# Optimization experiments

Measured on AMD Instinct MI355X. Metric: run time of the kernel, lower is better.

## Reference

```python
import jax, jax.numpy as jnp
import numpy as np

N_NODES = 10000
N_EDGES = 640000
D = 128


def setup_inputs() -> dict:
    key = jax.random.key(0)
    k1, k2, k3, k4 = jax.random.split(key, 4)
    X = jax.random.normal(k1, (N_NODES, D), dtype=jnp.float32)
    Y = jax.random.normal(k2, (N_EDGES, D), dtype=jnp.float32)
    # nn.Linear(in, out, bias=False): weight shape (out, in), y = Y @ W.T
    W = jax.random.normal(k3, (D, D), dtype=jnp.float32) * (1.0 / np.sqrt(D))
    edge_index = jax.random.randint(k4, (N_EDGES, 2), 0, N_NODES, dtype=jnp.int64)
    return {"X": X, "Y": Y, "W": W, "edge_index": edge_index}


def reference(X, Y, W, edge_index):
    # Edge transform: (E, d_in) @ (d_in, d_out) -> (E, d_out)
    Y_prime = jnp.einsum('ei,oi->eo', Y, W)
    # Scatter-add transformed edge features to source nodes
    src = edge_index[:, 0]
    agg = jax.ops.segment_sum(Y_prime, src, num_segments=X.shape[0])  # (N, d_out)
    # Residual + activation
    X_prime = jax.nn.relu(X + agg)
    return (X_prime, Y_prime)
```

## Files before the change

### kernel.cpp

```cpp
#include <hip/hip_runtime.h>

#define N_NODES 10000
#define N_EDGES 640000
#define DD 128
#define MAIN_BLOCKS 6250

typedef __attribute__((ext_vector_type(8))) short short8;
typedef __attribute__((ext_vector_type(8))) float f32x8;
typedef __attribute__((ext_vector_type(4))) float f32x4;
typedef __attribute__((ext_vector_type(2))) float f32x2;

__device__ __forceinline__ unsigned pack_bf2(float lo, float hi) {
  return __builtin_amdgcn_perm(__float_as_uint(hi), __float_as_uint(lo), 0x07060302u);
}

__device__ __forceinline__ void stage_w512(const float* __restrict__ W,
                                           short8* lwr) {
  const int tid = threadIdx.x;
#pragma unroll
  for (int t = 0; t < 4; ++t) {
    int s = t * 512 + tid;
    f32x8 v = *(const f32x8*)(W + (size_t)s * 8);
    short8 av;
    unsigned* au = (unsigned*)&av;
    au[0] = pack_bf2(v[0], v[1]);
    au[1] = pack_bf2(v[2], v[3]);
    au[2] = pack_bf2(v[4], v[5]);
    au[3] = pack_bf2(v[6], v[7]);
    int j = s >> 4;
    int c = s & 15;
    lwr[(j << 4) | (c ^ (j & 7))] = av;
  }
  __syncthreads();
}

__device__ __forceinline__ void stage_w256(const float* __restrict__ W,
                                           short8* lwr) {
  const int tid = threadIdx.x;
#pragma unroll
  for (int t = 0; t < 8; ++t) {
    int s = t * 256 + tid;
    f32x8 v = *(const f32x8*)(W + (size_t)s * 8);
    short8 av;
    unsigned* au = (unsigned*)&av;
    au[0] = pack_bf2(v[0], v[1]);
    au[1] = pack_bf2(v[2], v[3]);
    au[2] = pack_bf2(v[4], v[5]);
    au[3] = pack_bf2(v[6], v[7]);
    int j = s >> 4;
    int c = s & 15;
    lwr[(j << 4) | (c ^ (j & 7))] = av;
  }
  __syncthreads();
}

__global__ __launch_bounds__(256) void k_zero(int* __restrict__ count) {
  const int i = blockIdx.x * 256 + threadIdx.x;
  if (i < N_NODES) count[i] = 0;
}

__global__ __launch_bounds__(256) void k_hist(const int* __restrict__ EI,
                                              int* __restrict__ count) {
  const int e = blockIdx.x * 256 + threadIdx.x;
  atomicAdd(&count[EI[2 * e]], 1);
}

__global__ __launch_bounds__(1024) void k_scan(const int* __restrict__ count,
                                               int* __restrict__ rowptr,
                                               int* __restrict__ cursor) {
  __shared__ int part[1024];
  const int tid = threadIdx.x;
  const int base = tid * 10;
  int local[10];
  int s = 0;
#pragma unroll
  for (int i = 0; i < 10; ++i) {
    const int idx = base + i;
    const int v = (idx < N_NODES) ? count[idx] : 0;
    local[i] = s;
    s += v;
  }
  part[tid] = s;
  __syncthreads();
  for (int off = 1; off < 1024; off <<= 1) {
    int v = 0;
    if (tid >= off) v = part[tid - off];
    __syncthreads();
    if (tid >= off) part[tid] += v;
    __syncthreads();
  }
  const int excl = (tid > 0) ? part[tid - 1] : 0;
#pragma unroll
  for (int i = 0; i < 10; ++i) {
    const int idx = base + i;
    if (idx < N_NODES) {
      const int r = excl + local[i];
      rowptr[idx] = r;
      cursor[idx] = r;
    }
  }
  if (tid == 1023) rowptr[N_NODES] = part[1023];
}

__global__ __launch_bounds__(256) void k_fill(const int* __restrict__ EI,
                                              int* __restrict__ cursor,
                                              int* __restrict__ col) {
  const int e = blockIdx.x * 256 + threadIdx.x;
  const int s = EI[2 * e];
  const int pos = atomicAdd(&cursor[s], 1);
  col[pos] = e;
}

__global__ __launch_bounds__(512, 5) void k_main(
    const float* __restrict__ Y,
    const float* __restrict__ W,
    const int* __restrict__ rowptr,
    const int* __restrict__ col,
    float* __restrict__ Yp,
    float* __restrict__ segY) {
  __shared__ short8 lwr[2048];
  const int role = blockIdx.x % 5;
  const int grp  = blockIdx.x / 5;

  if (role == 0) {
    const int node = grp * 8 + (threadIdx.x >> 6);
    const int lane = threadIdx.x & 63;
    const size_t co = 2 * lane;
    const int b  = rowptr[node];
    const int en = rowptr[node + 1];

    f32x2 acc = (f32x2){0.f, 0.f};
    int i = b;
    for (; i + 16 <= en; i += 16) {
      f32x2 v0 = *(const f32x2*)(Y + (size_t)col[i]      * DD + co);
      f32x2 v1 = *(const f32x2*)(Y + (size_t)col[i + 1]  * DD + co);
      f32x2 v2 = *(const f32x2*)(Y + (size_t)col[i + 2]  * DD + co);
      f32x2 v3 = *(const f32x2*)(Y + (size_t)col[i + 3]  * DD + co);
      f32x2 v4 = *(const f32x2*)(Y + (size_t)col[i + 4]  * DD + co);
      f32x2 v5 = *(const f32x2*)(Y + (size_t)col[i + 5]  * DD + co);
      f32x2 v6 = *(const f32x2*)(Y + (size_t)col[i + 6]  * DD + co);
      f32x2 v7 = *(const f32x2*)(Y + (size_t)col[i + 7]  * DD + co);
      f32x2 v8 = *(const f32x2*)(Y + (size_t)col[i + 8]  * DD + co);
      f32x2 v9 = *(const f32x2*)(Y + (size_t)col[i + 9]  * DD + co);
      f32x2 va = *(const f32x2*)(Y + (size_t)col[i + 10] * DD + co);
      f32x2 vb = *(const f32x2*)(Y + (size_t)col[i + 11] * DD + co);
      f32x2 vc = *(const f32x2*)(Y + (size_t)col[i + 12] * DD + co);
      f32x2 vd = *(const f32x2*)(Y + (size_t)col[i + 13] * DD + co);
      f32x2 ve = *(const f32x2*)(Y + (size_t)col[i + 14] * DD + co);
      f32x2 vf = *(const f32x2*)(Y + (size_t)col[i + 15] * DD + co);
      acc += v0; acc += v1; acc += v2; acc += v3;
      acc += v4; acc += v5; acc += v6; acc += v7;
      acc += v8; acc += v9; acc += va; acc += vb;
      acc += vc; acc += vd; acc += ve; acc += vf;
    }
    for (; i < en; ++i) {
      acc += *(const f32x2*)(Y + (size_t)col[i] * DD + co);
    }
    *(f32x2*)(segY + (size_t)node * DD + co) = acc;
    return;
  }

  stage_w512(W, lwr);
  const int wid  = threadIdx.x >> 6;
  const int lane = threadIdx.x & 63;
  const int l15  = lane & 15;
  const int lg   = lane >> 4;
  const int koff = lg * 8;
  const int chunk = grp * 4 + (role - 1);
  const int row   = chunk * 128 + wid * 16 + l15;

  const float* yr = Y + (size_t)row * DD;
  short8 a[4];
#pragma unroll
  for (int kk = 0; kk < 4; ++kk) {
    f32x8 v = *(const f32x8*)(yr + kk * 32 + koff);
    short8 av;
    unsigned* au = (unsigned*)&av;
    au[0] = pack_bf2(v[0], v[1]);
    au[1] = pack_bf2(v[2], v[3]);
    au[2] = pack_bf2(v[4], v[5]);
    au[3] = pack_bf2(v[6], v[7]);
    a[kk] = av;
  }

  f32x4 acc[8];
#pragma unroll
  for (int nt = 0; nt < 8; ++nt)
    acc[nt] = (f32x4){0.f, 0.f, 0.f, 0.f};

#pragma unroll
  for (int nt = 0; nt < 8; ++nt) {
    const int j = nt * 16 + l15;
#pragma unroll
    for (int kk = 0; kk < 4; ++kk) {
      const int kc = kk * 4 + lg;
      short8 b = lwr[(j << 4) | (kc ^ (j & 7))];
      acc[nt] = __builtin_amdgcn_mfma_f32_16x16x32_bf16(b, a[kk], acc[nt], 0, 0, 0);
    }
  }

  float* orow = Yp + (size_t)row * DD + lg * 4;
#pragma unroll
  for (int nt = 0; nt < 8; ++nt)
    __builtin_nontemporal_store(acc[nt], (f32x4*)(orow + nt * 16));
}

__global__ __launch_bounds__(256, 2) void k_small(
    const float* __restrict__ segY,
    const float* __restrict__ W,
    const float* __restrict__ X,
    float* __restrict__ Xp) {
  __shared__ short8 lwr[2048];
  stage_w256(W, lwr);
  const int wid  = threadIdx.x >> 6;
  const int lane = threadIdx.x & 63;
  const int l15  = lane & 15;
  const int lg   = lane >> 4;
  const int koff = lg * 8;
  const int rbase = blockIdx.x * 128 + wid * 32;

  short8 a[2][4];
#pragma unroll
  for (int mt = 0; mt < 2; ++mt) {
    int row = rbase + mt * 16 + l15;
    if (row > N_NODES - 1) row = N_NODES - 1;
    const float* sr = segY + (size_t)row * DD + koff;
#pragma unroll
    for (int kk = 0; kk < 4; ++kk) {
      f32x8 v = *(const f32x8*)(sr + kk * 32);
      short8 av;
      unsigned* au = (unsigned*)&av;
      au[0] = pack_bf2(v[0], v[1]);
      au[1] = pack_bf2(v[2], v[3]);
      au[2] = pack_bf2(v[4], v[5]);
      au[3] = pack_bf2(v[6], v[7]);
      a[mt][kk] = av;
    }
  }

  f32x4 acc[2][8];
#pragma unroll
  for (int mt = 0; mt < 2; ++mt)
#pragma unroll
    for (int nt = 0; nt < 8; ++nt)
      acc[mt][nt] = (f32x4){0.f, 0.f, 0.f, 0.f};

#pragma unroll
  for (int nt = 0; nt < 8; ++nt) {
    const int j = nt * 16 + l15;
#pragma unroll
    for (int kk = 0; kk < 4; ++kk) {
      const int kc = kk * 4 + lg;
      short8 b = lwr[(j << 4) | (kc ^ (j & 7))];
      acc[0][nt] = __builtin_amdgcn_mfma_f32_16x16x32_bf16(b, a[0][kk], acc[0][nt], 0, 0, 0);
      acc[1][nt] = __builtin_amdgcn_mfma_f32_16x16x32_bf16(b, a[1][kk], acc[1][nt], 0, 0, 0);
    }
  }

#pragma unroll
  for (int mt = 0; mt < 2; ++mt) {
    const int row = rbase + mt * 16 + l15;
    if (row < N_NODES) {
      const float* xr   = X  + (size_t)row * DD + lg * 4;
      float*       orow = Xp + (size_t)row * DD + lg * 4;
#pragma unroll
      for (int nt = 0; nt < 8; ++nt) {
        f32x4 x = *(const f32x4*)(xr + nt * 16);
        f32x4 v = acc[mt][nt] + x;
        f32x4 r;
        r[0] = v[0] > 0.f ? v[0] : 0.f;
        r[1] = v[1] > 0.f ? v[1] : 0.f;
        r[2] = v[2] > 0.f ? v[2] : 0.f;
        r[3] = v[3] > 0.f ? v[3] : 0.f;
        *(f32x4*)(orow + nt * 16) = r;
      }
    }
  }
}

extern "C" void kernel_launch(void* const* d_in, const int* in_sizes, int n_in,
                              void* d_out, int out_size, void* d_ws, size_t ws_size,
                              hipStream_t stream) {
  const float* X  = (const float*)d_in[0];
  const float* Y  = (const float*)d_in[1];
  const float* W  = (const float*)d_in[2];
  const int*   EI = (const int*)d_in[3];

  float* Xp = (float*)d_out;
  float* Yp = Xp + (size_t)N_NODES * DD;

  int* w      = (int*)d_ws;
  int* count  = w;
  int* rowptr = w + 10000;
  int* cursor = w + 20001;
  int* col    = w + 30001;
  float* segY = (float*)(w + 670001 + 15);

  k_zero<<<(N_NODES + 255) / 256, 256, 0, stream>>>(count);
  k_hist<<<N_EDGES / 256, 256, 0, stream>>>(EI, count);
  k_scan<<<1, 1024, 0, stream>>>(count, rowptr, cursor);
  k_fill<<<N_EDGES / 256, 256, 0, stream>>>(EI, cursor, col);
  k_main<<<MAIN_BLOCKS, 512, 0, stream>>>(Y, W, rowptr, col, Yp, segY);
  k_small<<<(N_NODES + 127) / 128, 256, 0, stream>>>(segY, W, X, Xp);
}
```

Before: 298.3 us.

## Make k_main persistent with grid-stride loops and register prefetch of next Y tile

```diff
diff --git a/kernel.cpp b/kernel.cpp
--- a/kernel.cpp
+++ b/kernel.cpp
@@ -3,7 +3,10 @@
 #define N_NODES 10000
 #define N_EDGES 640000
 #define DD 128
-#define MAIN_BLOCKS 6250
+#define MAIN_BLOCKS 2560
+#define GEMM_COUNT 2048
+#define GATHER_WAVES 2048
+#define N_CHUNKS64 (N_EDGES / 64)
 
 typedef __attribute__((ext_vector_type(8))) short short8;
 typedef __attribute__((ext_vector_type(8))) float f32x8;
@@ -12,26 +15,6 @@
 
 __device__ __forceinline__ unsigned pack_bf2(float lo, float hi) {
   return __builtin_amdgcn_perm(__float_as_uint(hi), __float_as_uint(lo), 0x07060302u);
-}
-
-__device__ __forceinline__ void stage_w512(const float* __restrict__ W,
-                                           short8* lwr) {
-  const int tid = threadIdx.x;
-#pragma unroll
-  for (int t = 0; t < 4; ++t) {
-    int s = t * 512 + tid;
-    f32x8 v = *(const f32x8*)(W + (size_t)s * 8);
-    short8 av;
-    unsigned* au = (unsigned*)&av;
-    au[0] = pack_bf2(v[0], v[1]);
-    au[1] = pack_bf2(v[2], v[3]);
-    au[2] = pack_bf2(v[4], v[5]);
-    au[3] = pack_bf2(v[6], v[7]);
-    int j = s >> 4;
-    int c = s & 15;
-    lwr[(j << 4) | (c ^ (j & 7))] = av;
-  }
-  __syncthreads();
 }
 
 __device__ __forceinline__ void stage_w256(const float* __restrict__ W,
@@ -111,7 +94,7 @@
   col[pos] = e;
 }
 
-__global__ __launch_bounds__(512, 5) void k_main(
+__global__ __launch_bounds__(256, 4) void k_main(
     const float* __restrict__ Y,
     const float* __restrict__ W,
     const int* __restrict__ rowptr,
@@ -121,88 +104,117 @@
   __shared__ short8 lwr[2048];
   const int role = blockIdx.x % 5;
   const int grp  = blockIdx.x / 5;
-
-  if (role == 0) {
-    const int node = grp * 8 + (threadIdx.x >> 6);
-    const int lane = threadIdx.x & 63;
-    const size_t co = 2 * lane;
-    const int b  = rowptr[node];
-    const int en = rowptr[node + 1];
-
-    f32x2 acc = (f32x2){0.f, 0.f};
-    int i = b;
-    for (; i + 16 <= en; i += 16) {
-      f32x2 v0 = *(const f32x2*)(Y + (size_t)col[i]      * DD + co);
-      f32x2 v1 = *(const f32x2*)(Y + (size_t)col[i + 1]  * DD + co);
-      f32x2 v2 = *(const f32x2*)(Y + (size_t)col[i + 2]  * DD + co);
-      f32x2 v3 = *(const f32x2*)(Y + (size_t)col[i + 3]  * DD + co);
-      f32x2 v4 = *(const f32x2*)(Y + (size_t)col[i + 4]  * DD + co);
-      f32x2 v5 = *(const f32x2*)(Y + (size_t)col[i + 5]  * DD + co);
-      f32x2 v6 = *(const f32x2*)(Y + (size_t)col[i + 6]  * DD + co);
-      f32x2 v7 = *(const f32x2*)(Y + (size_t)col[i + 7]  * DD + co);
-      f32x2 v8 = *(const f32x2*)(Y + (size_t)col[i + 8]  * DD + co);
-      f32x2 v9 = *(const f32x2*)(Y + (size_t)col[i + 9]  * DD + co);
-      f32x2 va = *(const f32x2*)(Y + (size_t)col[i + 10] * DD + co);
-      f32x2 vb = *(const f32x2*)(Y + (size_t)col[i + 11] * DD + co);
-      f32x2 vc = *(const f32x2*)(Y + (size_t)col[i + 12] * DD + co);
-      f32x2 vd = *(const f32x2*)(Y + (size_t)col[i + 13] * DD + co);
-      f32x2 ve = *(const f32x2*)(Y + (size_t)col[i + 14] * DD + co);
-      f32x2 vf = *(const f32x2*)(Y + (size_t)col[i + 15] * DD + co);
-      acc += v0; acc += v1; acc += v2; acc += v3;
-      acc += v4; acc += v5; acc += v6; acc += v7;
-      acc += v8; acc += v9; acc += va; acc += vb;
-      acc += vc; acc += vd; acc += ve; acc += vf;
-    }
-    for (; i < en; ++i) {
-      acc += *(const f32x2*)(Y + (size_t)col[i] * DD + co);
-    }
-    *(f32x2*)(segY + (size_t)node * DD + co) = acc;
-    return;
-  }
-
-  stage_w512(W, lwr);
   const int wid  = threadIdx.x >> 6;
   const int lane = threadIdx.x & 63;
+
+  if (role == 0) {
+    const size_t co = 2 * (size_t)lane;
+#pragma unroll 1
+    for (int node = grp * 4 + wid; node < N_NODES; node += GATHER_WAVES) {
+      const int b  = rowptr[node];
+      const int en = rowptr[node + 1];
+      f32x2 acc = (f32x2){0.f, 0.f};
+      int i = b;
+      for (; i + 16 <= en; i += 16) {
+        f32x2 v0 = *(const f32x2*)(Y + (size_t)col[i]      * DD + co);
+        f32x2 v1 = *(const f32x2*)(Y + (size_t)col[i + 1]  * DD + co);
+        f32x2 v2 = *(const f32x2*)(Y + (size_t)col[i + 2]  * DD + co);
+        f32x2 v3 = *(const f32x2*)(Y + (size_t)col[i + 3]  * DD + co);
+        f32x2 v4 = *(const f32x2*)(Y + (size_t)col[i + 4]  * DD + co);
+        f32x2 v5 = *(const f32x2*)(Y + (size_t)col[i + 5]  * DD + co);
+        f32x2 v6 = *(const f32x2*)(Y + (size_t)col[i + 6]  * DD + co);
+        f32x2 v7 = *(const f32x2*)(Y + (size_t)col[i + 7]  * DD + co);
+        f32x2 v8 = *(const f32x2*)(Y + (size_t)col[i + 8]  * DD + co);
+        f32x2 v9 = *(const f32x2*)(Y + (size_t)col[i + 9]  * DD + co);
+        f32x2 va = *(const f32x2*)(Y + (size_t)col[i + 10] * DD + co);
+        f32x2 vb = *(const f32x2*)(Y + (size_t)col[i + 11] * DD + co);
+        f32x2 vc = *(const f32x2*)(Y + (size_t)col[i + 12] * DD + co);
+        f32x2 vd = *(const f32x2*)(Y + (size_t)col[i + 13] * DD + co);
+        f32x2 ve = *(const f32x2*)(Y + (size_t)col[i + 14] * DD + co);
+        f32x2 vf = *(const f32x2*)(Y + (size_t)col[i + 15] * DD + co);
+        acc += v0; acc += v1; acc += v2; acc += v3;
+        acc += v4; acc += v5; acc += v6; acc += v7;
+        acc += v8; acc += v9; acc += va; acc += vb;
+        acc += vc; acc += vd; acc += ve; acc += vf;
+      }
+      for (; i < en; ++i) {
+        acc += *(const f32x2*)(Y + (size_t)col[i] * DD + co);
+      }
+      *(f32x2*)(segY + (size_t)node * DD + co) = acc;
+    }
+    return;
+  }
+
+  stage_w256(W, lwr);
   const int l15  = lane & 15;
   const int lg   = lane >> 4;
   const int koff = lg * 8;
-  const int chunk = grp * 4 + (role - 1);
-  const int row   = chunk * 128 + wid * 16 + l15;
-
-  const float* yr = Y + (size_t)row * DD;
-  short8 a[4];
-#pragma unroll
-  for (int kk = 0; kk < 4; ++kk) {
-    f32x8 v = *(const f32x8*)(yr + kk * 32 + koff);
-    short8 av;
-    unsigned* au = (unsigned*)&av;
-    au[0] = pack_bf2(v[0], v[1]);
-    au[1] = pack_bf2(v[2], v[3]);
-    au[2] = pack_bf2(v[4], v[5]);
-    au[3] = pack_bf2(v[6], v[7]);
-    a[kk] = av;
-  }
-
-  f32x4 acc[8];
-#pragma unroll
-  for (int nt = 0; nt < 8; ++nt)
-    acc[nt] = (f32x4){0.f, 0.f, 0.f, 0.f};
-
-#pragma unroll
-  for (int nt = 0; nt < 8; ++nt) {
-    const int j = nt * 16 + l15;
+  const int gemm_id = grp * 4 + (role - 1);
+
+  f32x4 raw[8];
+  int c = gemm_id;
+
+  {
+    const float* yr = Y + (size_t)(c * 64 + wid * 16 + l15) * DD + koff;
 #pragma unroll
     for (int kk = 0; kk < 4; ++kk) {
-      const int kc = kk * 4 + lg;
-      short8 b = lwr[(j << 4) | (kc ^ (j & 7))];
-      acc[nt] = __builtin_amdgcn_mfma_f32_16x16x32_bf16(b, a[kk], acc[nt], 0, 0, 0);
-    }
-  }
-
-  float* orow = Yp + (size_t)row * DD + lg * 4;
-#pragma unroll
-  for (int nt = 0; nt < 8; ++nt)
-    __builtin_nontemporal_store(acc[nt], (f32x4*)(orow + nt * 16));
+      raw[kk * 2 + 0] = *(const f32x4*)(yr + kk * 32);
+      raw[kk * 2 + 1] = *(const f32x4*)(yr + kk * 32 + 4);
+    }
+  }
+
+#pragma unroll 1
+  while (true) {
+    const int row = c * 64 + wid * 16 + l15;
+    const int cn = c + GEMM_COUNT;
+
+    short8 a[4];
+#pragma unroll
+    for (int kk = 0; kk < 4; ++kk) {
+      f32x4 v0 = raw[kk * 2];
+      f32x4 v1 = raw[kk * 2 + 1];
+      short8 av;
+      unsigned* au = (unsigned*)&av;
+      au[0] = pack_bf2(v0[0], v0[1]);
+      au[1] = pack_bf2(v0[2], v0[3]);
+      au[2] = pack_bf2(v1[0], v1[1]);
+      au[3] = pack_bf2(v1[2], v1[3]);
+      a[kk] = av;
+    }
+
+    if (cn < N_CHUNKS64) {
+      const float* yr = Y + (size_t)(cn * 64 + wid * 16 + l15) * DD + koff;
+#pragma unroll
+      for (int kk = 0; kk < 4; ++kk) {
+        raw[kk * 2 + 0] = *(const f32x4*)(yr + kk * 32);
+        raw[kk * 2 + 1] = *(const f32x4*)(yr + kk * 32 + 4);
+      }
+    }
+
+    f32x4 acc[8];
+#pragma unroll
+    for (int nt = 0; nt < 8; ++nt)
+      acc[nt] = (f32x4){0.f, 0.f, 0.f, 0.f};
+
+#pragma unroll
+    for (int nt = 0; nt < 8; ++nt) {
+      const int j = nt * 16 + l15;
+#pragma unroll
+      for (int kk = 0; kk < 4; ++kk) {
+        const int kc = kk * 4 + lg;
+        short8 b = lwr[(j << 4) | (kc ^ (j & 7))];
+        acc[nt] = __builtin_amdgcn_mfma_f32_16x16x32_bf16(b, a[kk], acc[nt], 0, 0, 0);
+      }
+    }
+
+    float* orow = Yp + (size_t)row * DD + lg * 4;
+#pragma unroll
+    for (int nt = 0; nt < 8; ++nt)
+      __builtin_nontemporal_store(acc[nt], (f32x4*)(orow + nt * 16));
+
+    if (cn >= N_CHUNKS64) break;
+    c = cn;
+  }
 }
 
 __global__ __launch_bounds__(256, 2) void k_small(
@@ -300,6 +312,6 @@
   k_hist<<<N_EDGES / 256, 256, 0, stream>>>(EI, count);
   k_scan<<<1, 1024, 0, stream>>>(count, rowptr, cursor);
   k_fill<<<N_EDGES / 256, 256, 0, stream>>>(EI, cursor, col);
-  k_main<<<MAIN_BLOCKS, 512, 0, stream>>>(Y, W, rowptr, col, Yp, segY);
+  k_main<<<MAIN_BLOCKS, 256, 0, stream>>>(Y, W, rowptr, col, Yp, segY);
   k_small<<<(N_NODES + 127) / 128, 256, 0, stream>>>(segY, W, X, Xp);
 }
```

New measurement: 468.0 us. 56.9% more time.

## Fuse edge GEMM chunks into histogram and fill kernels to overlap CSR build

Applied to the files above, without the earlier changes.

```diff
diff --git a/kernel.cpp b/kernel.cpp
--- a/kernel.cpp
+++ b/kernel.cpp
@@ -3,7 +3,7 @@
 #define N_NODES 10000
 #define N_EDGES 640000
 #define DD 128
-#define MAIN_BLOCKS 6250
+#define MAIN_BLOCKS 7500
 
 typedef __attribute__((ext_vector_type(8))) short short8;
 typedef __attribute__((ext_vector_type(8))) float f32x8;
@@ -12,26 +12,6 @@
 
 __device__ __forceinline__ unsigned pack_bf2(float lo, float hi) {
   return __builtin_amdgcn_perm(__float_as_uint(hi), __float_as_uint(lo), 0x07060302u);
-}
-
-__device__ __forceinline__ void stage_w512(const float* __restrict__ W,
-                                           short8* lwr) {
-  const int tid = threadIdx.x;
-#pragma unroll
-  for (int t = 0; t < 4; ++t) {
-    int s = t * 512 + tid;
-    f32x8 v = *(const f32x8*)(W + (size_t)s * 8);
-    short8 av;
-    unsigned* au = (unsigned*)&av;
-    au[0] = pack_bf2(v[0], v[1]);
-    au[1] = pack_bf2(v[2], v[3]);
-    au[2] = pack_bf2(v[4], v[5]);
-    au[3] = pack_bf2(v[6], v[7]);
-    int j = s >> 4;
-    int c = s & 15;
-    lwr[(j << 4) | (c ^ (j & 7))] = av;
-  }
-  __syncthreads();
 }
 
 __device__ __forceinline__ void stage_w256(const float* __restrict__ W,
@@ -54,15 +34,66 @@
   __syncthreads();
 }
 
+__device__ __forceinline__ void gemm_chunk(const float* __restrict__ Y,
+                                           float* __restrict__ Yp,
+                                           const short8* lwr, int chunk) {
+  const int wid  = threadIdx.x >> 6;
+  const int lane = threadIdx.x & 63;
+  const int l15  = lane & 15;
+  const int lg   = lane >> 4;
+  const int koff = lg * 8;
+  const int row  = chunk * 64 + wid * 16 + l15;
+
+  const float* yr = Y + (size_t)row * DD;
+  short8 a[4];
+#pragma unroll
+  for (int kk = 0; kk < 4; ++kk) {
+    f32x8 v = *(const f32x8*)(yr + kk * 32 + koff);
+    short8 av;
+    unsigned* au = (unsigned*)&av;
+    au[0] = pack_bf2(v[0], v[1]);
+    au[1] = pack_bf2(v[2], v[3]);
+    au[2] = pack_bf2(v[4], v[5]);
+    au[3] = pack_bf2(v[6], v[7]);
+    a[kk] = av;
+  }
+
+  f32x4 acc[8];
+#pragma unroll
+  for (int nt = 0; nt < 8; ++nt)
+    acc[nt] = (f32x4){0.f, 0.f, 0.f, 0.f};
+
+#pragma unroll
+  for (int nt = 0; nt < 8; ++nt) {
+    const int j = nt * 16 + l15;
+#pragma unroll
+    for (int kk = 0; kk < 4; ++kk) {
+      const int kc = kk * 4 + lg;
+      short8 b = lwr[(j << 4) | (kc ^ (j & 7))];
+      acc[nt] = __builtin_amdgcn_mfma_f32_16x16x32_bf16(b, a[kk], acc[nt], 0, 0, 0);
+    }
+  }
+
+  float* orow = Yp + (size_t)row * DD + lg * 4;
+#pragma unroll
+  for (int nt = 0; nt < 8; ++nt)
+    __builtin_nontemporal_store(acc[nt], (f32x4*)(orow + nt * 16));
+}
+
 __global__ __launch_bounds__(256) void k_zero(int* __restrict__ count) {
   const int i = blockIdx.x * 256 + threadIdx.x;
   if (i < N_NODES) count[i] = 0;
 }
 
-__global__ __launch_bounds__(256) void k_hist(const int* __restrict__ EI,
-                                              int* __restrict__ count) {
+__global__ __launch_bounds__(256, 2) void k_hist_gemm(
+    const int* __restrict__ EI, int* __restrict__ count,
+    const float* __restrict__ Y, const float* __restrict__ W,
+    float* __restrict__ Yp) {
+  __shared__ short8 lwr[2048];
   const int e = blockIdx.x * 256 + threadIdx.x;
   atomicAdd(&count[EI[2 * e]], 1);
+  stage_w256(W, lwr);
+  gemm_chunk(Y, Yp, lwr, blockIdx.x);
 }
 
 __global__ __launch_bounds__(1024) void k_scan(const int* __restrict__ count,
@@ -102,16 +133,21 @@
   if (tid == 1023) rowptr[N_NODES] = part[1023];
 }
 
-__global__ __launch_bounds__(256) void k_fill(const int* __restrict__ EI,
-                                              int* __restrict__ cursor,
-                                              int* __restrict__ col) {
+__global__ __launch_bounds__(256, 2) void k_fill_gemm(
+    const int* __restrict__ EI, int* __restrict__ cursor,
+    int* __restrict__ col,
+    const float* __restrict__ Y, const float* __restrict__ W,
+    float* __restrict__ Yp) {
+  __shared__ short8 lwr[2048];
   const int e = blockIdx.x * 256 + threadIdx.x;
   const int s = EI[2 * e];
   const int pos = atomicAdd(&cursor[s], 1);
   col[pos] = e;
-}
-
-__global__ __launch_bounds__(512, 5) void k_main(
+  stage_w256(W, lwr);
+  gemm_chunk(Y, Yp, lwr, 2500 + blockIdx.x);
+}
+
+__global__ __launch_bounds__(256, 2) void k_main(
     const float* __restrict__ Y,
     const float* __restrict__ W,
     const int* __restrict__ rowptr,
@@ -119,16 +155,16 @@
     float* __restrict__ Yp,
     float* __restrict__ segY) {
   __shared__ short8 lwr[2048];
-  const int role = blockIdx.x % 5;
-  const int grp  = blockIdx.x / 5;
+  const int role = blockIdx.x % 3;
+  const int grp  = blockIdx.x / 3;
+  const int wid  = threadIdx.x >> 6;
+  const int lane = threadIdx.x & 63;
 
   if (role == 0) {
-    const int node = grp * 8 + (threadIdx.x >> 6);
-    const int lane = threadIdx.x & 63;
-    const size_t co = 2 * lane;
+    const int node = grp * 4 + wid;
+    const size_t co = 2 * (size_t)lane;
     const int b  = rowptr[node];
     const int en = rowptr[node + 1];
-
     f32x2 acc = (f32x2){0.f, 0.f};
     int i = b;
     for (; i + 16 <= en; i += 16) {
@@ -160,49 +196,8 @@
     return;
   }
 
-  stage_w512(W, lwr);
-  const int wid  = threadIdx.x >> 6;
-  const int lane = threadIdx.x & 63;
-  const int l15  = lane & 15;
-  const int lg   = lane >> 4;
-  const int koff = lg * 8;
-  const int chunk = grp * 4 + (role - 1);
-  const int row   = chunk * 128 + wid * 16 + l15;
-
-  const float* yr = Y + (size_t)row * DD;
-  short8 a[4];
-#pragma unroll
-  for (int kk = 0; kk < 4; ++kk) {
-    f32x8 v = *(const f32x8*)(yr + kk * 32 + koff);
-    short8 av;
-    unsigned* au = (unsigned*)&av;
-    au[0] = pack_bf2(v[0], v[1]);
-    au[1] = pack_bf2(v[2], v[3]);
-    au[2] = pack_bf2(v[4], v[5]);
-    au[3] = pack_bf2(v[6], v[7]);
-    a[kk] = av;
-  }
-
-  f32x4 acc[8];
-#pragma unroll
-  for (int nt = 0; nt < 8; ++nt)
-    acc[nt] = (f32x4){0.f, 0.f, 0.f, 0.f};
-
-#pragma unroll
-  for (int nt = 0; nt < 8; ++nt) {
-    const int j = nt * 16 + l15;
-#pragma unroll
-    for (int kk = 0; kk < 4; ++kk) {
-      const int kc = kk * 4 + lg;
-      short8 b = lwr[(j << 4) | (kc ^ (j & 7))];
-      acc[nt] = __builtin_amdgcn_mfma_f32_16x16x32_bf16(b, a[kk], acc[nt], 0, 0, 0);
-    }
-  }
-
-  float* orow = Yp + (size_t)row * DD + lg * 4;
-#pragma unroll
-  for (int nt = 0; nt < 8; ++nt)
-    __builtin_nontemporal_store(acc[nt], (f32x4*)(orow + nt * 16));
+  stage_w256(W, lwr);
+  gemm_chunk(Y, Yp, lwr, 5000 + grp * 2 + (role - 1));
 }
 
 __global__ __launch_bounds__(256, 2) void k_small(
@@ -297,9 +292,9 @@
   float* segY = (float*)(w + 670001 + 15);
 
   k_zero<<<(N_NODES + 255) / 256, 256, 0, stream>>>(count);
-  k_hist<<<N_EDGES / 256, 256, 0, stream>>>(EI, count);
+  k_hist_gemm<<<2500, 256, 0, stream>>>(EI, count, Y, W, Yp);
   k_scan<<<1, 1024, 0, stream>>>(count, rowptr, cursor);
-  k_fill<<<N_EDGES / 256, 256, 0, stream>>>(EI, cursor, col);
-  k_main<<<MAIN_BLOCKS, 512, 0, stream>>>(Y, W, rowptr, col, Yp, segY);
+  k_fill_gemm<<<2500, 256, 0, stream>>>(EI, cursor, col, Y, W, Yp);
+  k_main<<<MAIN_BLOCKS, 256, 0, stream>>>(Y, W, rowptr, col, Yp, segY);
   k_small<<<(N_NODES + 127) / 128, 256, 0, stream>>>(segY, W, X, Xp);
 }
```

Result: faster. 275.3 us, median of 2 (-7.7%).
